# Optimization experiments

Measured on AMD Instinct MI355X. Metric: run time of the kernel, lower is better.

## Reference

```python
import jax, jax.numpy as jnp
import numpy as np

SPATIAL = (14, 14)
FEATURE_DIM = 768
N, T, H, D = 16, 8, 12, 64
L = SPATIAL[0] * SPATIAL[1] + 1  # 197 (cls token + 196 patches)
W_SIZE = (2 * SPATIAL[0] - 1) * (2 * SPATIAL[1] - 1)  # 729


def _build_idx():
    # relative-position index map [196, 196], matches the torch double loop
    hs, ws = SPATIAL
    pos = np.arange(hs * ws)
    pi, pj = pos // ws, pos % ws
    i_offs = pi[:, None] - pi[None, :] + hs - 1
    j_offs = pj[:, None] - pj[None, :] + ws - 1
    return jnp.asarray(i_offs * (2 * ws - 1) + j_offs, dtype=jnp.int32)


def setup_inputs() -> dict:
    key = jax.random.key(0)
    kq, kk, kw1, kw2 = jax.random.split(key, 4)
    q = jax.random.normal(kq, (N, T, L, H, D), dtype=jnp.float32)
    k = jax.random.normal(kk, (N, T, L, H, D), dtype=jnp.float32)
    # learned relative-position bias tables (zeros in torch init; use small random for a meaningful baseline)
    w1 = jax.random.normal(kw1, (W_SIZE, FEATURE_DIM), dtype=jnp.float32) * 0.02
    w2 = jax.random.normal(kw2, (W_SIZE, FEATURE_DIM), dtype=jnp.float32) * 0.02
    idx = _build_idx()
    return {"q": q, "k": k, "w1": w1, "w2": w2, "idx": idx}


def _forward_half(q, k, w, idx):
    # q, k: [N, T', L, H, D]; strip cls token -> [N, T', 196, H, D]
    q = q[:, :, 1:]
    k = k[:, :, 1:]
    scale = 1.0 / jnp.sqrt(jnp.asarray(q.shape[-1], q.dtype))
    attn = jnp.einsum('ntqhd,ntkhd->ntqkh', q * scale, k)
    attn = jax.nn.softmax(attn, axis=-2).mean(axis=-1)  # [N, T', 196, 196]
    w_unroll = w[idx]  # gather: [196, 196, C]
    return jnp.einsum('ntqk,qkc->ntqc', attn, w_unroll)


def reference(q, k, w1, w2, idx):
    n, t, l, _, _ = q.shape
    c = w1.shape[-1]
    ret = jnp.zeros((n, t, l, c), dtype=q.dtype)
    ret = ret.at[:, 1:, 1:, :].add(_forward_half(q[:, 1:], k[:, :-1], w1, idx))
    ret = ret.at[:, :-1, 1:, :].add(_forward_half(q[:, :-1], k[:, 1:], w2, idx))
    return ret
```

## Files before the change

kernel.cpp:

```cpp
#include <hip/hip_runtime.h>

#define N_ 16
#define T_ 8
#define L_ 197
#define H_ 12
#define D_ 64
#define Q_ 196
#define C_ 768
#define KP 224
#define ENT 1792
#define ATS 216
#define APLANE 2112

typedef unsigned short ushort_t;
typedef __bf16 bf16x8 __attribute__((ext_vector_type(8)));
typedef float floatx4 __attribute__((ext_vector_type(4)));

#define GLD_LDS16(g, l)                                                    \
  __builtin_amdgcn_global_load_lds(                                        \
      (const __attribute__((address_space(1))) void*)(g),                  \
      (__attribute__((address_space(3))) void*)(l), 16, 0, 0)

static __device__ inline ushort_t f2bf(float x) {
  unsigned int u = __float_as_uint(x);
  u += 0x7fffu + ((u >> 16) & 1u);
  return (ushort_t)(u >> 16);
}
static __device__ inline unsigned int pack2(float a, float b) {
  return (unsigned int)f2bf(a) | ((unsigned int)f2bf(b) << 16);
}

__global__ __launch_bounds__(256) void convert_kernel(
    const float* __restrict__ q, const float* __restrict__ k,
    uint4* __restrict__ qb, uint4* __restrict__ kb) {
  const int nt  = blockIdx.x;
  const int pc  = blockIdx.y;
  const int inp = blockIdx.z;
  const int tid = threadIdx.x;
  const int pos0 = pc * 28;

  const float* src = inp ? k : q;
  const float sc = inp ? 1.f : 0.125f;
  uint4* dst = inp ? kb : qb;

  __shared__ uint2 lds[28][194];

  #pragma unroll
  for (int r = 0; r < 21; r++) {
    int e = tid + 256 * r;
    int row = e / 192, col = e - row * 192;
    float4 v = *(const float4*)(src + ((size_t)nt * L_ + 1 + pos0 + row) * (H_ * D_) + col * 4);
    uint2 p;
    p.x = pack2(v.x * sc, v.y * sc);
    p.y = pack2(v.z * sc, v.w * sc);
    lds[row][col] = p;
  }
  __syncthreads();

  #pragma unroll
  for (int r = 0; r < 11; r++) {
    int e = tid + 256 * r;
    if (e < 2688) {
      int hd = e / 28, p = e - hd * 28;
      uint2 a = lds[p][hd * 2];
      uint2 b = lds[p][hd * 2 + 1];
      int h = hd >> 3, dc = hd & 7;
      uint4 o; o.x = a.x; o.y = a.y; o.z = b.x; o.w = b.y;
      dst[((size_t)nt * H_ + h) * ENT + dc * KP + pos0 + p] = o;
    }
  }
}

__global__ __launch_bounds__(256, 4) void attn_kernel(
    const uint4* __restrict__ qb, const uint4* __restrict__ kb,
    ushort_t* __restrict__ A1, ushort_t* __restrict__ A2) {
  const int lin  = blockIdx.x;
  const int xcd  = lin & 7;
  const int slot = lin >> 3;
  const int g    = (slot >> 2) * 8 + xcd;
  const int b    = slot & 3;
  const int half = g / 112;
  const int nt   = g - half * 112;
  const int n  = nt / 7, tp = nt % 7;
  const int tq = (half == 0) ? tp + 1 : tp;
  const int tk = (half == 0) ? tp     : tp + 1;
  const int ntq = n * T_ + tq;
  const int ntk = n * T_ + tk;

  const uint4* qpl = qb + (size_t)ntq * H_ * ENT;
  const uint4* kpl = kb + (size_t)ntk * H_ * ENT;
  ushort_t* Ah = (half == 0) ? A1 : A2;

  __shared__ __align__(16) uint4 ks[ENT];
  ushort_t* at = (ushort_t*)ks;
  const ushort_t* ksu = (const ushort_t*)ks;

  const int tid  = threadIdx.x;
  const int lane = tid & 63;
  const int wv   = tid >> 6;
  const int quad = lane >> 4;
  const int l15  = lane & 15;
  const int qi_b = 64 * b + 16 * wv;

  float accA[13][4];
  #pragma unroll
  for (int t = 0; t < 13; t++)
    #pragma unroll
    for (int r = 0; r < 4; r++) accA[t][r] = 0.f;

  #pragma unroll
  for (int r = 0; r < 7; r++)
    GLD_LDS16(kpl + 256 * r + 64 * wv + lane, (char*)ks + (256 * r + 64 * wv) * 16);
  bf16x8 qf[2];
  #pragma unroll
  for (int kk = 0; kk < 2; kk++)
    qf[kk] = *(const bf16x8*)&qpl[(quad + 4 * kk) * KP + qi_b + l15];

  for (int h = 0; h < H_; h++) {
    __syncthreads();

    floatx4 S[13];
    #pragma unroll
    for (int t = 0; t < 13; t++) S[t] = (floatx4){0.f, 0.f, 0.f, 0.f};
    #pragma unroll
    for (int kk = 0; kk < 2; kk++)
      #pragma unroll
      for (int t = 0; t < 13; t++) {
        bf16x8 bbv = *(const bf16x8*)&ksu[((quad + 4 * kk) * KP + 16 * t + l15) * 8];
        S[t] = __builtin_amdgcn_mfma_f32_16x16x32_bf16(qf[kk], bbv, S[t], 0, 0, 0);
      }

    __syncthreads();
    if (h + 1 < H_) {
      #pragma unroll
      for (int kk = 0; kk < 2; kk++)
        qf[kk] = *(const bf16x8*)&qpl[(size_t)(h + 1) * ENT + (quad + 4 * kk) * KP + qi_b + l15];
      #pragma unroll
      for (int r = 0; r < 7; r++)
        GLD_LDS16(kpl + (size_t)(h + 1) * ENT + 256 * r + 64 * wv + lane,
                  (char*)ks + (256 * r + 64 * wv) * 16);
    }

    #pragma unroll
    for (int r = 0; r < 4; r++) {
      float s = 0.f;
      #pragma unroll
      for (int t = 0; t < 13; t++) {
        float e_ = (t == 12 && l15 >= 4) ? 0.f : __expf(S[t][r]);
        S[t][r] = e_;
        s += e_;
      }
      #pragma unroll
      for (int off = 1; off < 16; off <<= 1) s += __shfl_xor(s, off);
      float inv = 1.f / s;
      #pragma unroll
      for (int t = 0; t < 13; t++) accA[t][r] += S[t][r] * inv;
    }
  }

  const float s12 = 1.f / 12.f;
  #pragma unroll
  for (int t = 0; t < 13; t++)
    #pragma unroll
    for (int r = 0; r < 4; r++)
      at[(16 * wv + 4 * quad + r) * ATS + 16 * t + l15] = f2bf(accA[t][r] * s12);
  #pragma unroll
  for (int i = 0; i < 7; i++) {
    int e = lane + 64 * i;
    if (e < 416) {
      int row = e / 26, col = e - row * 26;
      uint4 v = *(const uint4*)&at[(16 * wv + row) * ATS + col * 8];
      int qi = qi_b + row;
      if (qi < Q_)
        *(uint4*)(Ah + ((size_t)qi * (N_ * T_) + ntq) * KP + col * 8) = v;
    }
  }
}

__global__ __launch_bounds__(256, 4) void mix_kernel(
    const ushort_t* __restrict__ A1, const ushort_t* __restrict__ A2,
    const float* __restrict__ w1, const float* __restrict__ w2,
    const int* __restrict__ idx, float* __restrict__ out) {
  const int ct = blockIdx.x;
  const int qi = blockIdx.y;
  const int tid  = threadIdx.x;
  const int lane = tid & 63;
  const int wv   = tid >> 6;
  const int quad = lane >> 4;
  const int l15  = lane & 15;
  const int p    = lane >> 2;
  const int cq   = lane & 3;

  __shared__ __align__(16) char As[2][4 * APLANE];
  __shared__ ushort_t Ws[128][40];

  int idxr0[7], idxr1[7];
  #pragma unroll
  for (int kc = 0; kc < 7; kc++) {
    int off = 32 * kc + 2 * p;
    if (off > 194) off = 194;
    int2 pr = *(const int2*)(idx + (size_t)qi * Q_ + off);
    idxr0[kc] = pr.x; idxr1[kc] = pr.y;
  }

  floatx4 acc[8][2];
  #pragma unroll
  for (int mt = 0; mt < 8; mt++)
    #pragma unroll
    for (int u = 0; u < 2; u++) acc[mt][u] = (floatx4){0.f, 0.f, 0.f, 0.f};

  float4 pw[2][2];
  const int cbase = ct * 128 + wv * 32;

  {
    const ushort_t* Ah_ = A1;
    #pragma unroll
    for (int r = 0; r < 2; r++)
      GLD_LDS16(Ah_ + ((size_t)qi * 128 + r * 64 + lane) * KP + wv * 8,
                As[0] + wv * APLANE + r * 1024);
    #pragma unroll
    for (int j = 0; j < 2; j++)
      #pragma unroll
      for (int u = 0; u < 2; u++)
        pw[j][u] = *(const float4*)(w1 + (size_t)(j ? idxr1[0] : idxr0[0]) * C_ +
                                    cbase + (cq + 4 * u) * 4);
  }

  #pragma unroll
  for (int ht = 0; ht < 14; ht++) {
    const int half = ht / 7, kc = ht % 7;
    __syncthreads();

    #pragma unroll
    for (int u = 0; u < 2; u++) {
      const float* f0 = (const float*)&pw[0][u];
      const float* f1 = (const float*)&pw[1][u];
      #pragma unroll
      for (int e = 0; e < 4; e++)
        *(unsigned int*)&Ws[wv * 32 + (cq + 4 * u) * 4 + e][2 * p] = pack2(f0[e], f1[e]);
    }

    if (ht + 1 < 14) {
      const int nh = (ht + 1) / 7, nk = (ht + 1) % 7;
      const ushort_t* Ah_ = nh ? A2 : A1;
      const float* w_ = nh ? w2 : w1;
      #pragma unroll
      for (int r = 0; r < 2; r++)
        GLD_LDS16(Ah_ + ((size_t)qi * 128 + r * 64 + lane) * KP + 32 * nk + wv * 8,
                  As[(ht + 1) & 1] + wv * APLANE + r * 1024);
      int r0 = idxr0[nk], r1 = idxr1[nk];
      #pragma unroll
      for (int u = 0; u < 2; u++) {
        pw[0][u] = *(const float4*)(w_ + (size_t)r0 * C_ + cbase + (cq + 4 * u) * 4);
        pw[1][u] = *(const float4*)(w_ + (size_t)r1 * C_ + cbase + (cq + 4 * u) * 4);
      }
    }

    const char* ab = As[ht & 1];
    bf16x8 bfv[2];
    #pragma unroll
    for (int u = 0; u < 2; u++)
      bfv[u] = *(const bf16x8*)&Ws[wv * 32 + 16 * u + l15][8 * quad];
    #pragma unroll
    for (int mt = 0; mt < 8; mt++) {
      bf16x8 a = *(const bf16x8*)(ab + quad * APLANE + (16 * mt + l15) * 16);
      acc[mt][0] = __builtin_amdgcn_mfma_f32_16x16x32_bf16(a, bfv[0], acc[mt][0], 0, 0, 0);
      acc[mt][1] = __builtin_amdgcn_mfma_f32_16x16x32_bf16(a, bfv[1], acc[mt][1], 0, 0, 0);
    }
  }

  #pragma unroll
  for (int u = 0; u < 2; u++) {
    const int c = ct * 128 + 32 * wv + 16 * u + l15;
    #pragma unroll
    for (int mt = 0; mt < 8; mt++)
      #pragma unroll
      for (int r = 0; r < 4; r++) {
        int m = 16 * mt + 4 * quad + r;
        out[((size_t)m * L_ + 1 + qi) * C_ + c] = acc[mt][u][r];
      }
  }
  if (qi == 0) {
    #pragma unroll
    for (int u = 0; u < 2; u++) {
      const int c = ct * 128 + 32 * wv + 16 * u + l15;
      #pragma unroll
      for (int mt = 0; mt < 8; mt++)
        #pragma unroll
        for (int r = 0; r < 4; r++) {
          int m = 16 * mt + 4 * quad + r;
          out[(size_t)m * L_ * C_ + c] = 0.f;
        }
    }
  }
}

extern "C" void kernel_launch(void* const* d_in, const int* in_sizes, int n_in,
                              void* d_out, int out_size, void* d_ws, size_t ws_size,
                              hipStream_t stream) {
  const float* q  = (const float*)d_in[0];
  const float* k  = (const float*)d_in[1];
  const float* w1 = (const float*)d_in[2];
  const float* w2 = (const float*)d_in[3];
  const int* idx  = (const int*)d_in[4];
  float* out = (float*)d_out;

  const size_t plane_tot = (size_t)(N_ * T_) * H_ * ENT;
  uint4* qb = (uint4*)d_ws;
  uint4* kb = qb + plane_tot;
  ushort_t* A1 = (ushort_t*)(kb + plane_tot);
  size_t Aelems = (size_t)Q_ * (N_ * T_) * KP;
  ushort_t* A2 = A1 + Aelems;

  hipMemsetAsync(A1, 0, Aelems * 2 * sizeof(ushort_t), stream);

  convert_kernel<<<dim3(N_ * T_, 7, 2), 256, 0, stream>>>(q, k, qb, kb);
  attn_kernel<<<dim3(896), 256, 0, stream>>>(qb, kb, A1, A2);
  mix_kernel<<<dim3(6, Q_), 256, 0, stream>>>(A1, A2, w1, w2, idx, out);
}
```

Baseline: 405.4 us.

## Double-buffer K tiles in LDS to prefetch two heads ahead

Replaces the single K buffer in the attention kernel with two LDS buffers. Loads for head h+2 are issued while head h+1's data is still in flight, and waits use explicit vmcnt counts instead of full syncthreads. The goal is to hide global-to-LDS latency between heads. In exchange, LDS use per block doubles and launch bounds drop from 4 to 2 blocks per SM, which lowers occupancy. The hand-written waitcnt values are also fragile.

```diff
diff --git a/kernel.cpp b/kernel.cpp
--- a/kernel.cpp
+++ b/kernel.cpp
@@ -71,7 +71,7 @@
   }
 }
 
-__global__ __launch_bounds__(256, 4) void attn_kernel(
+__global__ __launch_bounds__(256, 2) void attn_kernel(
     const uint4* __restrict__ qb, const uint4* __restrict__ kb,
     ushort_t* __restrict__ A1, ushort_t* __restrict__ A2) {
   const int lin  = blockIdx.x;
@@ -91,9 +91,8 @@
   const uint4* kpl = kb + (size_t)ntk * H_ * ENT;
   ushort_t* Ah = (half == 0) ? A1 : A2;
 
-  __shared__ __align__(16) uint4 ks[ENT];
+  __shared__ __align__(16) uint4 ks[2][ENT];
   ushort_t* at = (ushort_t*)ks;
-  const ushort_t* ksu = (const ushort_t*)ks;
 
   const int tid  = threadIdx.x;
   const int lane = tid & 63;
@@ -108,17 +107,25 @@
     #pragma unroll
     for (int r = 0; r < 4; r++) accA[t][r] = 0.f;
 
-  #pragma unroll
-  for (int r = 0; r < 7; r++)
-    GLD_LDS16(kpl + 256 * r + 64 * wv + lane, (char*)ks + (256 * r + 64 * wv) * 16);
-  bf16x8 qf[2];
-  #pragma unroll
-  for (int kk = 0; kk < 2; kk++)
-    qf[kk] = *(const bf16x8*)&qpl[(quad + 4 * kk) * KP + qi_b + l15];
-
-  for (int h = 0; h < H_; h++) {
-    __syncthreads();
-
+  auto stage = [&](int h, uint4* bufp) {
+    #pragma unroll
+    for (int r = 0; r < 7; r++)
+      GLD_LDS16(kpl + (size_t)h * ENT + 256 * r + 64 * wv + lane,
+                (char*)bufp + (256 * r + 64 * wv) * 16);
+  };
+  auto loadq = [&](int h, bf16x8* qf) {
+    #pragma unroll
+    for (int kk = 0; kk < 2; kk++)
+      qf[kk] = *(const bf16x8*)&qpl[(size_t)h * ENT + (quad + 4 * kk) * KP + qi_b + l15];
+  };
+
+  auto headbody = [&](int h, uint4* bufp, bf16x8* qf, bool lastwait) {
+    if (lastwait) asm volatile("s_waitcnt vmcnt(0)" ::: "memory");
+    else          asm volatile("s_waitcnt vmcnt(9)" ::: "memory");
+    __builtin_amdgcn_s_barrier();
+    asm volatile("" ::: "memory");
+
+    const ushort_t* bu = (const ushort_t*)bufp;
     floatx4 S[13];
     #pragma unroll
     for (int t = 0; t < 13; t++) S[t] = (floatx4){0.f, 0.f, 0.f, 0.f};
@@ -126,19 +133,16 @@
     for (int kk = 0; kk < 2; kk++)
       #pragma unroll
       for (int t = 0; t < 13; t++) {
-        bf16x8 bbv = *(const bf16x8*)&ksu[((quad + 4 * kk) * KP + 16 * t + l15) * 8];
+        bf16x8 bbv = *(const bf16x8*)&bu[((quad + 4 * kk) * KP + 16 * t + l15) * 8];
         S[t] = __builtin_amdgcn_mfma_f32_16x16x32_bf16(qf[kk], bbv, S[t], 0, 0, 0);
       }
 
-    __syncthreads();
-    if (h + 1 < H_) {
-      #pragma unroll
-      for (int kk = 0; kk < 2; kk++)
-        qf[kk] = *(const bf16x8*)&qpl[(size_t)(h + 1) * ENT + (quad + 4 * kk) * KP + qi_b + l15];
-      #pragma unroll
-      for (int r = 0; r < 7; r++)
-        GLD_LDS16(kpl + (size_t)(h + 1) * ENT + 256 * r + 64 * wv + lane,
-                  (char*)ks + (256 * r + 64 * wv) * 16);
+    asm volatile("" ::: "memory");
+    __builtin_amdgcn_s_barrier();
+    if (h + 2 < H_) {
+      loadq(h + 2, qf);
+      stage(h + 2, bufp);
+      __builtin_amdgcn_sched_barrier(0);
     }
 
     #pragma unroll
@@ -156,6 +160,18 @@
       #pragma unroll
       for (int t = 0; t < 13; t++) accA[t][r] += S[t][r] * inv;
     }
+  };
+
+  bf16x8 qfA[2], qfB[2];
+  loadq(0, qfA); stage(0, ks[0]);
+  __builtin_amdgcn_sched_barrier(0);
+  loadq(1, qfB); stage(1, ks[1]);
+  __builtin_amdgcn_sched_barrier(0);
+
+  #pragma unroll 1
+  for (int hh = 0; hh < 6; hh++) {
+    headbody(2 * hh,     ks[0], qfA, false);
+    headbody(2 * hh + 1, ks[1], qfB, hh == 5);
   }
 
   const float s12 = 1.f / 12.f;
```

Result: faster. 340.5 us (-16.0%).
